# Performance work log

Hardware: AMD Instinct MI355X
Metric: run time of the kernel (lower is better)

The kernel has to match this reference:

```python
import jax, jax.numpy as jnp
import numpy as np
import math

B, N, D, K = 4, 255, 256, 128
NODE_FEATURES_OFFSET = 128
MAX_Z = 101
NUM_EDGES = 2 * NODE_FEATURES_OFFSET + 1  # 257
NUM_DIR_KERNEL = 128  # FourierDirectionalEmbed num_kernel
ECFG_F = 20  # synthetic electron-config feature dim


def setup_inputs() -> dict:
    key = jax.random.key(0)
    ks = jax.random.split(key, 16)
    positions = jax.random.normal(ks[0], (B, N, 3), dtype=jnp.float32) * 3.0
    atomic_numbers = jax.random.randint(ks[1], (B, N), 1, MAX_Z, dtype=jnp.int32)
    s = 0.02
    emb_z = jax.random.normal(ks[2], (MAX_Z + 1, D), dtype=jnp.float32) * s
    electron_config = jax.random.uniform(ks[3], (MAX_Z + 1, ECFG_F), dtype=jnp.float32)
    config_W = jax.random.normal(ks[4], (ECFG_F, D), dtype=jnp.float32) * s
    config_b = jnp.zeros((D,), dtype=jnp.float32)
    mult_W = jax.random.normal(ks[5], (NODE_FEATURES_OFFSET, D), dtype=jnp.float32) * s
    charge_W = jax.random.normal(ks[6], (NODE_FEATURES_OFFSET, D), dtype=jnp.float32) * s
    gbf_means = jax.random.uniform(ks[7], (K,), dtype=jnp.float32, minval=0.0, maxval=7.0)
    gbf_stds = jax.random.uniform(ks[8], (K,), dtype=jnp.float32, minval=0.0, maxval=3.0)
    gbf_mul = jax.random.normal(ks[9], (NUM_EDGES,), dtype=jnp.float32).at[0].set(0.0)  # padding_idx=0
    gbf_bias = (jax.random.normal(ks[10], (NUM_EDGES,), dtype=jnp.float32) * 0.1).at[0].set(0.0)
    proj1_W = jax.random.normal(ks[11], (K, K), dtype=jnp.float32) * (1.0 / math.sqrt(K))
    proj1_b = jnp.zeros((K,), dtype=jnp.float32)
    proj2_W = jax.random.normal(ks[12], (K, D), dtype=jnp.float32) * (1.0 / math.sqrt(K))
    proj2_b = jnp.zeros((D,), dtype=jnp.float32)
    dir_W = jax.random.normal(ks[13], (2 * NUM_DIR_KERNEL, D), dtype=jnp.float32) * (1.0 / math.sqrt(2 * NUM_DIR_KERNEL))
    dir_b = jnp.zeros((D,), dtype=jnp.float32)
    return dict(positions=positions, atomic_numbers=atomic_numbers, emb_z=emb_z,
                electron_config=electron_config, config_W=config_W, config_b=config_b,
                mult_W=mult_W, charge_W=charge_W, gbf_means=gbf_means, gbf_stds=gbf_stds,
                gbf_mul=gbf_mul, gbf_bias=gbf_bias, proj1_W=proj1_W, proj1_b=proj1_b,
                proj2_W=proj2_W, proj2_b=proj2_b, dir_W=dir_W, dir_b=dir_b)


def _angular_freqs():
    min_angle = 1e-4
    half = NUM_DIR_KERNEL // 2
    wl_az = jnp.exp(jnp.linspace(math.log(2 * min_angle), math.log(2 * 2 * math.pi), half))
    wl_po = jnp.exp(jnp.linspace(math.log(2 * min_angle), math.log(2 * math.pi), half))
    return (2 * math.pi / wl_az).astype(jnp.float32), (2 * math.pi / wl_po).astype(jnp.float32)


def _forward(positions, atomic_numbers, emb_z, electron_config, config_W, config_b,
             mult_W, charge_W, gbf_means, gbf_stds, gbf_mul, gbf_bias,
             proj1_W, proj1_b, proj2_W, proj2_b, dir_W, dir_b):
    b = positions.shape[0]
    # add graph-level (CLS) token: zero position, z = MAX_Z = 101
    pos = jnp.concatenate([jnp.zeros_like(positions[:, :1]), positions], axis=1)  # [B,Np,3]
    z = jnp.concatenate([jnp.full_like(atomic_numbers[:, :1], MAX_Z), atomic_numbers], axis=1)  # [B,Np]
    npad = pos.shape[1]

    # --- node embedding: nuclear + electronic + multiplicity(1) + charge(0) ---
    elec = electron_config[z] @ config_W + config_b            # [B,Np,D]
    elec = elec.at[:, 0, :].set(0.0)                            # cls_token row zeroed
    node = emb_z[z] + elec + mult_W[1] + charge_W[0]           # [B,Np,D]

    # --- pairwise geometry: directions[b,i,j] = pos[j] - pos[i] ---
    d = pos[:, None, :, :] - pos[:, :, None, :]                # [B,Np,Np,3]
    sq = jnp.sum(d * d, axis=-1)
    dist = jnp.sqrt(sq + 1e-12)                                # [B,Np,Np]
    nd = d / (dist[..., None] + 1e-5)                          # normed directions, eps per source
    eye = jnp.eye(npad, dtype=bool)[None, :, :]
    x_safe = jnp.where(eye, 1.0, nd[..., 0])
    y_safe = jnp.where(eye, 0.0, nd[..., 1])
    azimuth = jnp.arctan2(y_safe, x_safe)                      # [B,Np,Np]
    polar = jnp.arccos(jnp.clip(nd[..., 2], -1.0 + 1e-6, 1.0 - 1e-6))

    # --- FourierDirectionalEmbed ---
    f_az, f_po = _angular_freqs()
    ph_az = azimuth[..., None] * f_az                          # [B,Np,Np,64]
    ph_po = polar[..., None] * f_po
    sinusoids = jnp.concatenate([jnp.sin(ph_az), jnp.cos(ph_az),
                                 jnp.sin(ph_po), jnp.cos(ph_po)], axis=-1)  # [B,Np,Np,256]
    dir_out = sinusoids @ dir_W + dir_b                        # [B,Np,Np,D]

    # --- Gaussian3DEmbed ---
    zi = z[:, :, None]
    zj = z[:, None, :] + NODE_FEATURES_OFFSET
    mul = gbf_mul[zi] + gbf_mul[zj]                            # sum over the 2 edge-type entries
    bias = gbf_bias[zi] + gbf_bias[zj]                         # [B,Np,Np]
    gx = (mul * dist + bias)[..., None]                        # [B,Np,Np,1] -> broadcast to K
    std = jnp.abs(gbf_stds) + 0.01
    pi_c = 3.14159
    gauss = jnp.exp(-0.5 * ((gx - gbf_means) / std) ** 2) / ((2 * pi_c) ** 0.5 * std)  # [B,Np,Np,K]
    h = jax.nn.gelu(gauss @ proj1_W + proj1_b, approximate=False)
    gbf_out = h @ proj2_W + proj2_b                            # [B,Np,Np,D]

    return node, gbf_out, dir_out


def reference(positions, atomic_numbers, emb_z, electron_config, config_W, config_b,
              mult_W, charge_W, gbf_means, gbf_stds, gbf_mul, gbf_bias,
              proj1_W, proj1_b, proj2_W, proj2_b, dir_W, dir_b):
    return _forward(positions, atomic_numbers, emb_z, electron_config, config_W, config_b,
                    mult_W, charge_W, gbf_means, gbf_stds, gbf_mul, gbf_bias,
                    proj1_W, proj1_b, proj2_W, proj2_b, dir_W, dir_b)
```

## Files before the change

### kernel.cpp

```cpp
#include <hip/hip_runtime.h>
#include <math.h>

typedef __bf16 bf16x8 __attribute__((ext_vector_type(8)));
typedef __bf16 bf16x4 __attribute__((ext_vector_type(4)));
typedef float f32x4 __attribute__((ext_vector_type(4)));
typedef float f32x2 __attribute__((ext_vector_type(2)));

#define PI_D 3.14159265358979323846
#define IH 0.15915494f
#define IL 6.4206383e-9f

__device__ __forceinline__ void bar_lds() {
  __builtin_amdgcn_sched_barrier(0);
  asm volatile("s_waitcnt lgkmcnt(0)" ::: "memory");
  __builtin_amdgcn_s_barrier();
  __builtin_amdgcn_sched_barrier(0);
}

__global__ void prep_kernel(const float* __restrict__ dir_W,
                            const float* __restrict__ proj1_W,
                            const float* __restrict__ proj2_W,
                            const float* __restrict__ gbf_stds,
                            const float* __restrict__ gbf_means,
                            __bf16* __restrict__ dirP, __bf16* __restrict__ p1P,
                            __bf16* __restrict__ p2P,
                            float* __restrict__ f_az, float* __restrict__ f_po,
                            f32x2* __restrict__ gAB, float* __restrict__ gcoef) {
  int tid = threadIdx.x + blockIdx.x * blockDim.x;
  int nth = gridDim.x * blockDim.x;
  for (int o8 = tid; o8 < 8192; o8 += nth) {
    int l = o8 & 63, ks = (o8 >> 6) & 7, nt = o8 >> 9;
    int d = nt * 16 + (l & 15);
    int s0 = ks * 32 + (l >> 4) * 8;
    bf16x8 v;
#pragma unroll
    for (int j = 0; j < 8; ++j) v[j] = (__bf16)dir_W[(s0 + j) * 256 + d];
    *(bf16x8*)(dirP + o8 * 8) = v;
  }
  for (int o8 = tid; o8 < 2048; o8 += nth) {
    int l = o8 & 63, ks = (o8 >> 6) & 3, nt = o8 >> 8;
    int ko = nt * 16 + (l & 15);
    int k0 = ks * 32 + (l >> 4) * 8;
    bf16x8 v;
#pragma unroll
    for (int j = 0; j < 8; ++j) v[j] = (__bf16)proj1_W[(k0 + j) * 128 + ko];
    *(bf16x8*)(p1P + o8 * 8) = v;
  }
  for (int o8 = tid; o8 < 4096; o8 += nth) {
    int l = o8 & 63, ks = (o8 >> 6) & 3, nt = o8 >> 8;
    int d = nt * 16 + (l & 15);
    int k0 = ks * 32 + (l >> 4) * 8;
    bf16x8 v;
#pragma unroll
    for (int j = 0; j < 8; ++j) v[j] = (__bf16)proj2_W[(k0 + j) * 256 + d];
    *(bf16x8*)(p2P + o8 * 8) = v;
  }
  if (blockIdx.x == 0 && threadIdx.x < 64) {
    int q = threadIdx.x;
    double l0 = log(2.0 * 1e-4);
    double l1a = log(2.0 * 2.0 * PI_D);
    double l1p = log(2.0 * PI_D);
    double ta = l0 + (l1a - l0) * (double)q / 63.0;
    double tp = l0 + (l1p - l0) * (double)q / 63.0;
    f_az[q] = (float)(2.0 * PI_D / exp(ta));
    f_po[q] = (float)(2.0 * PI_D / exp(tp));
  }
  if (blockIdx.x == 1 && threadIdx.x < 128) {
    int k = threadIdx.x;
    double sd = (double)(fabsf(gbf_stds[k]) + 0.01f);
    double c = sqrt(0.7213475204444817);
    double A = c / sd;
    f32x2 ab;
    ab.x = (float)A;
    ab.y = (float)(-A * (double)gbf_means[k]);
    gAB[k] = ab;
    gcoef[k] = (float)(1.0 / (sqrt(2.0 * 3.14159) * sd));
  }
}

__global__ void node_kernel(const int* __restrict__ an, const float* __restrict__ emb_z,
                            const float* __restrict__ ec, const float* __restrict__ cW,
                            const float* __restrict__ cb, const float* __restrict__ mult_W,
                            const float* __restrict__ charge_W, float* __restrict__ out_node) {
  int bi = blockIdx.x;
  int b = bi >> 8, i = bi & 255;
  int d = threadIdx.x;
  int z = (i == 0) ? 101 : an[b * 255 + i - 1];
  float elec = 0.0f;
  if (i != 0) {
    for (int f = 0; f < 20; ++f) elec += ec[z * 20 + f] * cW[f * 256 + d];
    elec += cb[d];
  }
  float v = emb_z[z * 256 + d] + elec + mult_W[256 + d] + charge_W[d];
  __builtin_nontemporal_store(v, &out_node[(size_t)bi * 256 + d]);
}

__global__ __launch_bounds__(256, 4) void pair_kernel(
    const float* __restrict__ positions, const int* __restrict__ atomic_numbers,
    const float* __restrict__ gbf_mul, const float* __restrict__ gbf_bias,
    const float* __restrict__ proj1_b, const float* __restrict__ proj2_b,
    const float* __restrict__ dir_b, const __bf16* __restrict__ dirP,
    const __bf16* __restrict__ p1P, const __bf16* __restrict__ p2P,
    const float* __restrict__ f_az, const float* __restrict__ f_po,
    const f32x2* __restrict__ gAB, const float* __restrict__ gcoef,
    float* __restrict__ out_gbf, float* __restrict__ out_dir) {
  __shared__ __align__(16) __bf16 buf[64 * 136];
  __shared__ float s_az[64], s_po[64], s_gx[64];

  const int tid = threadIdx.x;
  const int bid = blockIdx.x;
  const int jt = bid & 3;
  const int i = (bid >> 2) & 255;
  const int b = bid >> 10;
  const int j0 = jt * 64;
  const long pairbase = ((long)(b * 256 + i)) * 256 + j0;

  const int lane = tid & 63, wv = tid >> 6;
  const int lr = lane & 15, kb = lane >> 4;

  const int q8 = (tid & 7) * 8;
  const int pr2 = tid >> 3;
  const int k0g = (tid & 15) * 8;
  const int prow = tid >> 4;

  if (tid < 64) {
    int p = tid, j = j0 + p;
    float pxi = 0.f, pyi = 0.f, pzi = 0.f, pxj = 0.f, pyj = 0.f, pzj = 0.f;
    if (i != 0) { const float* q = positions + ((size_t)b * 255 + (i - 1)) * 3; pxi = q[0]; pyi = q[1]; pzi = q[2]; }
    if (j != 0) { const float* q = positions + ((size_t)b * 255 + (j - 1)) * 3; pxj = q[0]; pyj = q[1]; pzj = q[2]; }
    float dx = pxj - pxi, dy = pyj - pyi, dz = pzj - pzi;
    float sq = dx * dx + dy * dy + dz * dz;
    float dist = sqrtf(sq + 1e-12f);
    float inv = 1.0f / (dist + 1e-5f);
    float ndx = dx * inv, ndy = dy * inv, ndz = dz * inv;
    bool diag = (i == j);
    float xs = diag ? 1.0f : ndx;
    float ys = diag ? 0.0f : ndy;
    s_az[p] = atan2f(ys, xs);
    float cz = fminf(fmaxf(ndz, -1.0f + 1e-6f), 1.0f - 1e-6f);
    s_po[p] = acosf(cz);
    int zi = (i == 0) ? 101 : atomic_numbers[b * 255 + i - 1];
    int zj = ((j == 0) ? 101 : atomic_numbers[b * 255 + j - 1]) + 128;
    float mul = gbf_mul[zi] + gbf_mul[zj];
    float bia = gbf_bias[zi] + gbf_bias[zj];
    s_gx[p] = mul * dist + bia;
  }
  bar_lds();

  f32x4 acc[4][4];
#pragma unroll
  for (int mtl = 0; mtl < 4; ++mtl)
#pragma unroll
    for (int np = 0; np < 4; ++np) acc[mtl][np] = (f32x4){0.f, 0.f, 0.f, 0.f};

  for (int half = 0; half < 2; ++half) {
    const float* ft = half ? f_po : f_az;
    float fv[8];
#pragma unroll
    for (int t = 0; t < 8; ++t) fv[t] = ft[q8 + t];
#pragma unroll
    for (int it = 0; it < 2; ++it) {
      int p = pr2 + it * 32;
      float ang = half ? s_po[p] : s_az[p];
      bf16x8 sv, cv;
#pragma unroll
      for (int t = 0; t < 8; ++t) {
        float ph = ang * fv[t];
        float n = __builtin_rintf(ph * IH);
        float fr = __builtin_fmaf(ph, IH, -n) + ph * IL;
        sv[t] = (__bf16)__builtin_amdgcn_sinf(fr);
        cv[t] = (__bf16)__builtin_amdgcn_cosf(fr);
      }
      *(bf16x8*)(buf + p * 136 + q8) = sv;
      *(bf16x8*)(buf + p * 136 + 64 + q8) = cv;
    }
    bar_lds();
#pragma unroll
    for (int ksl = 0; ksl < 4; ++ksl) {
      int ks = half * 4 + ksl;
      bf16x8 bfr[4];
#pragma unroll
      for (int np = 0; np < 4; ++np)
        bfr[np] = *(const bf16x8*)(buf + (np * 16 + lr) * 136 + ksl * 32 + kb * 8);
#pragma unroll
      for (int mtl = 0; mtl < 4; ++mtl) {
        int mtile = mtl * 4 + wv;
        bf16x8 af = *(const bf16x8*)(dirP + (((size_t)mtile * 8 + ks) * 64 + lane) * 8);
#pragma unroll
        for (int np = 0; np < 4; ++np)
          acc[mtl][np] = __builtin_amdgcn_mfma_f32_16x16x32_bf16(af, bfr[np], acc[mtl][np], 0, 0, 0);
      }
    }
    bar_lds();
  }

  f32x2 abv[8];
  float gcv[8];
#pragma unroll
  for (int t = 0; t < 8; ++t) { abv[t] = gAB[k0g + t]; gcv[t] = gcoef[k0g + t]; }

#pragma unroll
  for (int mtl = 0; mtl < 4; ++mtl) {
    int dcol0 = (mtl * 4 + wv) * 16 + kb * 4;
    f32x4 bias = *(const f32x4*)(dir_b + dcol0);
#pragma unroll
    for (int np = 0; np < 4; ++np) {
      f32x4 v = acc[mtl][np] + bias;
      __builtin_nontemporal_store(v, (f32x4*)(out_dir + (pairbase + np * 16 + lr) * 256 + dcol0));
    }
  }

#pragma unroll
  for (int it = 0; it < 4; ++it) {
    int p = prow + it * 16;
    float gx = s_gx[p];
    bf16x8 gv;
#pragma unroll
    for (int t = 0; t < 8; ++t) {
      float y = __builtin_fmaf(gx, abv[t].x, abv[t].y);
      gv[t] = (__bf16)(exp2f(-y * y) * gcv[t]);
    }
    *(bf16x8*)(buf + p * 136 + k0g) = gv;
  }
  bar_lds();

  f32x4 acc1[2][4];
#pragma unroll
  for (int mtl = 0; mtl < 2; ++mtl)
#pragma unroll
    for (int np = 0; np < 4; ++np) acc1[mtl][np] = (f32x4){0.f, 0.f, 0.f, 0.f};
#pragma unroll
  for (int ksl = 0; ksl < 4; ++ksl) {
    bf16x8 bfr[4];
#pragma unroll
    for (int np = 0; np < 4; ++np)
      bfr[np] = *(const bf16x8*)(buf + (np * 16 + lr) * 136 + ksl * 32 + kb * 8);
#pragma unroll
    for (int mtl = 0; mtl < 2; ++mtl) {
      int mtile = mtl * 4 + wv;
      bf16x8 af = *(const bf16x8*)(p1P + (((size_t)mtile * 4 + ksl) * 64 + lane) * 8);
#pragma unroll
      for (int np = 0; np < 4; ++np)
        acc1[mtl][np] = __builtin_amdgcn_mfma_f32_16x16x32_bf16(af, bfr[np], acc1[mtl][np], 0, 0, 0);
    }
  }
  bar_lds();

#pragma unroll
  for (int mtl = 0; mtl < 2; ++mtl) {
    int ko0 = (mtl * 4 + wv) * 16 + kb * 4;
    f32x4 pb = *(const f32x4*)(proj1_b + ko0);
#pragma unroll
    for (int np = 0; np < 4; ++np) {
      f32x4 hv = acc1[mtl][np] + pb;
      bf16x4 hb;
#pragma unroll
      for (int r = 0; r < 4; ++r) {
        float v = hv[r];
        v = 0.5f * v * (1.0f + erff(v * 0.70710678118654752f));
        hb[r] = (__bf16)v;
      }
      *(bf16x4*)(buf + (np * 16 + lr) * 136 + ko0) = hb;
    }
  }
  bar_lds();

  f32x4 acc2[4][4];
#pragma unroll
  for (int mtl = 0; mtl < 4; ++mtl)
#pragma unroll
    for (int np = 0; np < 4; ++np) acc2[mtl][np] = (f32x4){0.f, 0.f, 0.f, 0.f};
#pragma unroll
  for (int ksl = 0; ksl < 4; ++ksl) {
    bf16x8 bfr[4];
#pragma unroll
    for (int np = 0; np < 4; ++np)
      bfr[np] = *(const bf16x8*)(buf + (np * 16 + lr) * 136 + ksl * 32 + kb * 8);
#pragma unroll
    for (int mtl = 0; mtl < 4; ++mtl) {
      int mtile = mtl * 4 + wv;
      bf16x8 af = *(const bf16x8*)(p2P + (((size_t)mtile * 4 + ksl) * 64 + lane) * 8);
#pragma unroll
      for (int np = 0; np < 4; ++np)
        acc2[mtl][np] = __builtin_amdgcn_mfma_f32_16x16x32_bf16(af, bfr[np], acc2[mtl][np], 0, 0, 0);
    }
  }
#pragma unroll
  for (int mtl = 0; mtl < 4; ++mtl) {
    int dcol0 = (mtl * 4 + wv) * 16 + kb * 4;
    f32x4 bias = *(const f32x4*)(proj2_b + dcol0);
#pragma unroll
    for (int np = 0; np < 4; ++np) {
      f32x4 v = acc2[mtl][np] + bias;
      __builtin_nontemporal_store(v, (f32x4*)(out_gbf + (pairbase + np * 16 + lr) * 256 + dcol0));
    }
  }
}

extern "C" void kernel_launch(void* const* d_in, const int* in_sizes, int n_in,
                              void* d_out, int out_size, void* d_ws, size_t ws_size,
                              hipStream_t stream) {
  const float* positions = (const float*)d_in[0];
  const int* atomic_numbers = (const int*)d_in[1];
  const float* emb_z = (const float*)d_in[2];
  const float* electron_config = (const float*)d_in[3];
  const float* config_W = (const float*)d_in[4];
  const float* config_b = (const float*)d_in[5];
  const float* mult_W = (const float*)d_in[6];
  const float* charge_W = (const float*)d_in[7];
  const float* gbf_means = (const float*)d_in[8];
  const float* gbf_stds = (const float*)d_in[9];
  const float* gbf_mul = (const float*)d_in[10];
  const float* gbf_bias = (const float*)d_in[11];
  const float* proj1_W = (const float*)d_in[12];
  const float* proj1_b = (const float*)d_in[13];
  const float* proj2_W = (const float*)d_in[14];
  const float* proj2_b = (const float*)d_in[15];
  const float* dir_W = (const float*)d_in[16];
  const float* dir_b = (const float*)d_in[17];

  float* out = (float*)d_out;
  float* out_node = out;
  float* out_gbf = out + 262144;
  float* out_dir = out + 262144 + 67108864;

  char* ws = (char*)d_ws;
  __bf16* dirP = (__bf16*)(ws);
  __bf16* p1P = (__bf16*)(ws + 131072);
  __bf16* p2P = (__bf16*)(ws + 163840);
  float* f_az = (float*)(ws + 229376);
  float* f_po = (float*)(ws + 229376 + 256);
  f32x2* gAB = (f32x2*)(ws + 229376 + 512);
  float* gcoef = (float*)(ws + 229376 + 1536);

  prep_kernel<<<64, 256, 0, stream>>>(dir_W, proj1_W, proj2_W, gbf_stds, gbf_means,
                                      dirP, p1P, p2P, f_az, f_po, gAB, gcoef);
  node_kernel<<<1024, 256, 0, stream>>>(atomic_numbers, emb_z, electron_config,
                                        config_W, config_b, mult_W, charge_W, out_node);
  pair_kernel<<<4096, 256, 0, stream>>>(positions, atomic_numbers, gbf_mul, gbf_bias,
                                        proj1_b, proj2_b, dir_b, dirP, p1P, p2P,
                                        f_az, f_po, gAB, gcoef, out_gbf, out_dir);
}
```

Baseline: 157.8 us.

## Process two pair tiles per block and alternate dir/gbf order across blocks

Halves the grid so each block handles two 64-pair tiles, hoisting the frequency and Gaussian coefficient loads and the per-tile geometry setup out of the per-tile loop. Odd blocks run the Gaussian MLP path before the directional path, so co-resident blocks hit different phases (transcendental-heavy vs MFMA/store-heavy) at the same time and contend less for the same units. It adds an extra barrier in the gbf path, and the larger per-block work may reduce load balance and raise register pressure.

```diff
diff --git a/kernel.cpp b/kernel.cpp
--- a/kernel.cpp
+++ b/kernel.cpp
@@ -105,26 +105,30 @@
     const f32x2* __restrict__ gAB, const float* __restrict__ gcoef,
     float* __restrict__ out_gbf, float* __restrict__ out_dir) {
   __shared__ __align__(16) __bf16 buf[64 * 136];
-  __shared__ float s_az[64], s_po[64], s_gx[64];
+  __shared__ float s_az[2][64], s_po[2][64], s_gx[2][64];
 
   const int tid = threadIdx.x;
   const int bid = blockIdx.x;
-  const int jt = bid & 3;
-  const int i = (bid >> 2) & 255;
-  const int b = bid >> 10;
-  const int j0 = jt * 64;
-  const long pairbase = ((long)(b * 256 + i)) * 256 + j0;
-
   const int lane = tid & 63, wv = tid >> 6;
   const int lr = lane & 15, kb = lane >> 4;
-
   const int q8 = (tid & 7) * 8;
   const int pr2 = tid >> 3;
   const int k0g = (tid & 15) * 8;
   const int prow = tid >> 4;
 
-  if (tid < 64) {
-    int p = tid, j = j0 + p;
+  float fva[8], fvp[8];
+#pragma unroll
+  for (int t = 0; t < 8; ++t) { fva[t] = f_az[q8 + t]; fvp[t] = f_po[q8 + t]; }
+  f32x2 abv[8];
+  float gcv[8];
+#pragma unroll
+  for (int t = 0; t < 8; ++t) { abv[t] = gAB[k0g + t]; gcv[t] = gcoef[k0g + t]; }
+
+  if (tid < 128) {
+    int p = tid & 63, u = tid >> 6;
+    int tile = bid + (u << 11);
+    int jt = tile & 3, i = (tile >> 2) & 255, b = tile >> 10;
+    int j = jt * 64 + p;
     float pxi = 0.f, pyi = 0.f, pzi = 0.f, pxj = 0.f, pyj = 0.f, pzj = 0.f;
     if (i != 0) { const float* q = positions + ((size_t)b * 255 + (i - 1)) * 3; pxi = q[0]; pyi = q[1]; pzi = q[2]; }
     if (j != 0) { const float* q = positions + ((size_t)b * 255 + (j - 1)) * 3; pxj = q[0]; pyj = q[1]; pzj = q[2]; }
@@ -136,164 +140,165 @@
     bool diag = (i == j);
     float xs = diag ? 1.0f : ndx;
     float ys = diag ? 0.0f : ndy;
-    s_az[p] = atan2f(ys, xs);
+    s_az[u][p] = atan2f(ys, xs);
     float cz = fminf(fmaxf(ndz, -1.0f + 1e-6f), 1.0f - 1e-6f);
-    s_po[p] = acosf(cz);
+    s_po[u][p] = acosf(cz);
     int zi = (i == 0) ? 101 : atomic_numbers[b * 255 + i - 1];
     int zj = ((j == 0) ? 101 : atomic_numbers[b * 255 + j - 1]) + 128;
     float mul = gbf_mul[zi] + gbf_mul[zj];
     float bia = gbf_bias[zi] + gbf_bias[zj];
-    s_gx[p] = mul * dist + bia;
+    s_gx[u][p] = mul * dist + bia;
   }
   bar_lds();
 
-  f32x4 acc[4][4];
-#pragma unroll
-  for (int mtl = 0; mtl < 4; ++mtl)
-#pragma unroll
-    for (int np = 0; np < 4; ++np) acc[mtl][np] = (f32x4){0.f, 0.f, 0.f, 0.f};
-
-  for (int half = 0; half < 2; ++half) {
-    const float* ft = half ? f_po : f_az;
-    float fv[8];
-#pragma unroll
-    for (int t = 0; t < 8; ++t) fv[t] = ft[q8 + t];
-#pragma unroll
-    for (int it = 0; it < 2; ++it) {
-      int p = pr2 + it * 32;
-      float ang = half ? s_po[p] : s_az[p];
-      bf16x8 sv, cv;
-#pragma unroll
-      for (int t = 0; t < 8; ++t) {
-        float ph = ang * fv[t];
-        float n = __builtin_rintf(ph * IH);
-        float fr = __builtin_fmaf(ph, IH, -n) + ph * IL;
-        sv[t] = (__bf16)__builtin_amdgcn_sinf(fr);
-        cv[t] = (__bf16)__builtin_amdgcn_cosf(fr);
-      }
-      *(bf16x8*)(buf + p * 136 + q8) = sv;
-      *(bf16x8*)(buf + p * 136 + 64 + q8) = cv;
-    }
-    bar_lds();
-#pragma unroll
-    for (int ksl = 0; ksl < 4; ++ksl) {
-      int ks = half * 4 + ksl;
-      bf16x8 bfr[4];
-#pragma unroll
-      for (int np = 0; np < 4; ++np)
-        bfr[np] = *(const bf16x8*)(buf + (np * 16 + lr) * 136 + ksl * 32 + kb * 8);
+  for (int u = 0; u < 2; ++u) {
+    const int tile = bid + (u << 11);
+    const int jt = tile & 3, i = (tile >> 2) & 255, b = tile >> 10;
+    const long pairbase = ((long)(b * 256 + i)) * 256 + jt * 64;
+
+    auto do_dir = [&]() {
+      f32x4 acc[4][4];
+#pragma unroll
+      for (int mtl = 0; mtl < 4; ++mtl)
+#pragma unroll
+        for (int np = 0; np < 4; ++np) acc[mtl][np] = (f32x4){0.f, 0.f, 0.f, 0.f};
+#pragma unroll
+      for (int half = 0; half < 2; ++half) {
+#pragma unroll
+        for (int it = 0; it < 2; ++it) {
+          int p = pr2 + it * 32;
+          float ang = half ? s_po[u][p] : s_az[u][p];
+          bf16x8 sv, cv;
+#pragma unroll
+          for (int t = 0; t < 8; ++t) {
+            float ph = ang * (half ? fvp[t] : fva[t]);
+            float n = __builtin_rintf(ph * IH);
+            float fr = __builtin_fmaf(ph, IH, -n) + ph * IL;
+            sv[t] = (__bf16)__builtin_amdgcn_sinf(fr);
+            cv[t] = (__bf16)__builtin_amdgcn_cosf(fr);
+          }
+          *(bf16x8*)(buf + p * 136 + q8) = sv;
+          *(bf16x8*)(buf + p * 136 + 64 + q8) = cv;
+        }
+        bar_lds();
+#pragma unroll
+        for (int ksl = 0; ksl < 4; ++ksl) {
+          int ks = half * 4 + ksl;
+          bf16x8 bfr[4];
+#pragma unroll
+          for (int np = 0; np < 4; ++np)
+            bfr[np] = *(const bf16x8*)(buf + (np * 16 + lr) * 136 + ksl * 32 + kb * 8);
+#pragma unroll
+          for (int mtl = 0; mtl < 4; ++mtl) {
+            int mtile = mtl * 4 + wv;
+            bf16x8 af = *(const bf16x8*)(dirP + (((size_t)mtile * 8 + ks) * 64 + lane) * 8);
+#pragma unroll
+            for (int np = 0; np < 4; ++np)
+              acc[mtl][np] = __builtin_amdgcn_mfma_f32_16x16x32_bf16(af, bfr[np], acc[mtl][np], 0, 0, 0);
+          }
+        }
+        bar_lds();
+      }
 #pragma unroll
       for (int mtl = 0; mtl < 4; ++mtl) {
-        int mtile = mtl * 4 + wv;
-        bf16x8 af = *(const bf16x8*)(dirP + (((size_t)mtile * 8 + ks) * 64 + lane) * 8);
+        int dcol0 = (mtl * 4 + wv) * 16 + kb * 4;
+        f32x4 bias = *(const f32x4*)(dir_b + dcol0);
+#pragma unroll
+        for (int np = 0; np < 4; ++np) {
+          f32x4 v = acc[mtl][np] + bias;
+          __builtin_nontemporal_store(v, (f32x4*)(out_dir + (pairbase + np * 16 + lr) * 256 + dcol0));
+        }
+      }
+    };
+
+    auto do_gbf = [&]() {
+#pragma unroll
+      for (int it = 0; it < 4; ++it) {
+        int p = prow + it * 16;
+        float gx = s_gx[u][p];
+        bf16x8 gv;
+#pragma unroll
+        for (int t = 0; t < 8; ++t) {
+          float y = __builtin_fmaf(gx, abv[t].x, abv[t].y);
+          gv[t] = (__bf16)(exp2f(-y * y) * gcv[t]);
+        }
+        *(bf16x8*)(buf + p * 136 + k0g) = gv;
+      }
+      bar_lds();
+      f32x4 acc1[2][4];
+#pragma unroll
+      for (int mtl = 0; mtl < 2; ++mtl)
+#pragma unroll
+        for (int np = 0; np < 4; ++np) acc1[mtl][np] = (f32x4){0.f, 0.f, 0.f, 0.f};
+#pragma unroll
+      for (int ksl = 0; ksl < 4; ++ksl) {
+        bf16x8 bfr[4];
 #pragma unroll
         for (int np = 0; np < 4; ++np)
-          acc[mtl][np] = __builtin_amdgcn_mfma_f32_16x16x32_bf16(af, bfr[np], acc[mtl][np], 0, 0, 0);
-      }
-    }
-    bar_lds();
-  }
-
-  f32x2 abv[8];
-  float gcv[8];
-#pragma unroll
-  for (int t = 0; t < 8; ++t) { abv[t] = gAB[k0g + t]; gcv[t] = gcoef[k0g + t]; }
-
-#pragma unroll
-  for (int mtl = 0; mtl < 4; ++mtl) {
-    int dcol0 = (mtl * 4 + wv) * 16 + kb * 4;
-    f32x4 bias = *(const f32x4*)(dir_b + dcol0);
-#pragma unroll
-    for (int np = 0; np < 4; ++np) {
-      f32x4 v = acc[mtl][np] + bias;
-      __builtin_nontemporal_store(v, (f32x4*)(out_dir + (pairbase + np * 16 + lr) * 256 + dcol0));
-    }
-  }
-
-#pragma unroll
-  for (int it = 0; it < 4; ++it) {
-    int p = prow + it * 16;
-    float gx = s_gx[p];
-    bf16x8 gv;
-#pragma unroll
-    for (int t = 0; t < 8; ++t) {
-      float y = __builtin_fmaf(gx, abv[t].x, abv[t].y);
-      gv[t] = (__bf16)(exp2f(-y * y) * gcv[t]);
-    }
-    *(bf16x8*)(buf + p * 136 + k0g) = gv;
-  }
-  bar_lds();
-
-  f32x4 acc1[2][4];
-#pragma unroll
-  for (int mtl = 0; mtl < 2; ++mtl)
-#pragma unroll
-    for (int np = 0; np < 4; ++np) acc1[mtl][np] = (f32x4){0.f, 0.f, 0.f, 0.f};
-#pragma unroll
-  for (int ksl = 0; ksl < 4; ++ksl) {
-    bf16x8 bfr[4];
-#pragma unroll
-    for (int np = 0; np < 4; ++np)
-      bfr[np] = *(const bf16x8*)(buf + (np * 16 + lr) * 136 + ksl * 32 + kb * 8);
-#pragma unroll
-    for (int mtl = 0; mtl < 2; ++mtl) {
-      int mtile = mtl * 4 + wv;
-      bf16x8 af = *(const bf16x8*)(p1P + (((size_t)mtile * 4 + ksl) * 64 + lane) * 8);
-#pragma unroll
-      for (int np = 0; np < 4; ++np)
-        acc1[mtl][np] = __builtin_amdgcn_mfma_f32_16x16x32_bf16(af, bfr[np], acc1[mtl][np], 0, 0, 0);
-    }
-  }
-  bar_lds();
-
-#pragma unroll
-  for (int mtl = 0; mtl < 2; ++mtl) {
-    int ko0 = (mtl * 4 + wv) * 16 + kb * 4;
-    f32x4 pb = *(const f32x4*)(proj1_b + ko0);
-#pragma unroll
-    for (int np = 0; np < 4; ++np) {
-      f32x4 hv = acc1[mtl][np] + pb;
-      bf16x4 hb;
-#pragma unroll
-      for (int r = 0; r < 4; ++r) {
-        float v = hv[r];
-        v = 0.5f * v * (1.0f + erff(v * 0.70710678118654752f));
-        hb[r] = (__bf16)v;
-      }
-      *(bf16x4*)(buf + (np * 16 + lr) * 136 + ko0) = hb;
-    }
-  }
-  bar_lds();
-
-  f32x4 acc2[4][4];
-#pragma unroll
-  for (int mtl = 0; mtl < 4; ++mtl)
-#pragma unroll
-    for (int np = 0; np < 4; ++np) acc2[mtl][np] = (f32x4){0.f, 0.f, 0.f, 0.f};
-#pragma unroll
-  for (int ksl = 0; ksl < 4; ++ksl) {
-    bf16x8 bfr[4];
-#pragma unroll
-    for (int np = 0; np < 4; ++np)
-      bfr[np] = *(const bf16x8*)(buf + (np * 16 + lr) * 136 + ksl * 32 + kb * 8);
-#pragma unroll
-    for (int mtl = 0; mtl < 4; ++mtl) {
-      int mtile = mtl * 4 + wv;
-      bf16x8 af = *(const bf16x8*)(p2P + (((size_t)mtile * 4 + ksl) * 64 + lane) * 8);
-#pragma unroll
-      for (int np = 0; np < 4; ++np)
-        acc2[mtl][np] = __builtin_amdgcn_mfma_f32_16x16x32_bf16(af, bfr[np], acc2[mtl][np], 0, 0, 0);
-    }
-  }
-#pragma unroll
-  for (int mtl = 0; mtl < 4; ++mtl) {
-    int dcol0 = (mtl * 4 + wv) * 16 + kb * 4;
-    f32x4 bias = *(const f32x4*)(proj2_b + dcol0);
-#pragma unroll
-    for (int np = 0; np < 4; ++np) {
-      f32x4 v = acc2[mtl][np] + bias;
-      __builtin_nontemporal_store(v, (f32x4*)(out_gbf + (pairbase + np * 16 + lr) * 256 + dcol0));
-    }
+          bfr[np] = *(const bf16x8*)(buf + (np * 16 + lr) * 136 + ksl * 32 + kb * 8);
+#pragma unroll
+        for (int mtl = 0; mtl < 2; ++mtl) {
+          int mtile = mtl * 4 + wv;
+          bf16x8 af = *(const bf16x8*)(p1P + (((size_t)mtile * 4 + ksl) * 64 + lane) * 8);
+#pragma unroll
+          for (int np = 0; np < 4; ++np)
+            acc1[mtl][np] = __builtin_amdgcn_mfma_f32_16x16x32_bf16(af, bfr[np], acc1[mtl][np], 0, 0, 0);
+        }
+      }
+      bar_lds();
+#pragma unroll
+      for (int mtl = 0; mtl < 2; ++mtl) {
+        int ko0 = (mtl * 4 + wv) * 16 + kb * 4;
+        f32x4 pb = *(const f32x4*)(proj1_b + ko0);
+#pragma unroll
+        for (int np = 0; np < 4; ++np) {
+          f32x4 hv = acc1[mtl][np] + pb;
+          bf16x4 hb;
+#pragma unroll
+          for (int r = 0; r < 4; ++r) {
+            float v = hv[r];
+            v = 0.5f * v * (1.0f + erff(v * 0.70710678118654752f));
+            hb[r] = (__bf16)v;
+          }
+          *(bf16x4*)(buf + (np * 16 + lr) * 136 + ko0) = hb;
+        }
+      }
+      bar_lds();
+      f32x4 acc2[4][4];
+#pragma unroll
+      for (int mtl = 0; mtl < 4; ++mtl)
+#pragma unroll
+        for (int np = 0; np < 4; ++np) acc2[mtl][np] = (f32x4){0.f, 0.f, 0.f, 0.f};
+#pragma unroll
+      for (int ksl = 0; ksl < 4; ++ksl) {
+        bf16x8 bfr[4];
+#pragma unroll
+        for (int np = 0; np < 4; ++np)
+          bfr[np] = *(const bf16x8*)(buf + (np * 16 + lr) * 136 + ksl * 32 + kb * 8);
+#pragma unroll
+        for (int mtl = 0; mtl < 4; ++mtl) {
+          int mtile = mtl * 4 + wv;
+          bf16x8 af = *(const bf16x8*)(p2P + (((size_t)mtile * 4 + ksl) * 64 + lane) * 8);
+#pragma unroll
+          for (int np = 0; np < 4; ++np)
+            acc2[mtl][np] = __builtin_amdgcn_mfma_f32_16x16x32_bf16(af, bfr[np], acc2[mtl][np], 0, 0, 0);
+        }
+      }
+      bar_lds();
+#pragma unroll
+      for (int mtl = 0; mtl < 4; ++mtl) {
+        int dcol0 = (mtl * 4 + wv) * 16 + kb * 4;
+        f32x4 bias = *(const f32x4*)(proj2_b + dcol0);
+#pragma unroll
+        for (int np = 0; np < 4; ++np) {
+          f32x4 v = acc2[mtl][np] + bias;
+          __builtin_nontemporal_store(v, (f32x4*)(out_gbf + (pairbase + np * 16 + lr) * 256 + dcol0));
+        }
+      }
+    };
+
+    if ((bid & 1) == 0) { do_dir(); do_gbf(); }
+    else                { do_gbf(); do_dir(); }
   }
 }
 
@@ -337,7 +342,7 @@
                                       dirP, p1P, p2P, f_az, f_po, gAB, gcoef);
   node_kernel<<<1024, 256, 0, stream>>>(atomic_numbers, emb_z, electron_config,
                                         config_W, config_b, mult_W, charge_W, out_node);
-  pair_kernel<<<4096, 256, 0, stream>>>(positions, atomic_numbers, gbf_mul, gbf_bias,
+  pair_kernel<<<2048, 256, 0, stream>>>(positions, atomic_numbers, gbf_mul, gbf_bias,
                                         proj1_b, proj2_b, dir_b, dirP, p1P, p2P,
                                         f_az, f_po, gAB, gcoef, out_gbf, out_dir);
 }
```

New measurement: 257.7 us. 63.3% more time.
